# Kernel optimization log

Measured on AMD Instinct MI355X. Metric: run time of the kernel, lower is better.

Reference implementation:

```python
import jax, jax.numpy as jnp
import numpy as np

BS = 256          # batch_size
NN = BS - 1
D = 128           # projection dim
SIGMA = 0.07      # rbf gamma (self.sigma)
C = 1.0
REG = 0.1
NUM_ITERS = 1000
ETA = 0.001
USE_NORM = True


def setup_inputs() -> dict:
    key = jax.random.key(0)
    k1, k2 = jax.random.split(key)
    z = jax.random.normal(k1, (BS, 2, D), dtype=jnp.float32)
    alpha_init = jax.random.normal(k2, (BS, NN, 1), dtype=jnp.float32)
    return {"z": z, "alpha_init": alpha_init}


def _rbf_kernel(X, Y, gamma):
    # exp(-gamma * ||x - y||^2)
    xn = jnp.sum(X * X, axis=1, keepdims=True)          # [n,1]
    yn = jnp.sum(Y * Y, axis=1, keepdims=True).T        # [1,m]
    d = xn + yn - 2.0 * (X @ Y.T)
    return jnp.exp(-gamma * d)


def _pgd_nesterov(DD, p, alpha0, eta, num_iters, C, use_norm):
    # minimize 0.5 a'DDa - p'a  s.t. 0 <= a <= C, batched over bs
    def step(carry, t):
        alpha, alpha_prev = carry
        beta = t / (t + 3.0)
        y = alpha + beta * (alpha - alpha_prev)
        grad = jnp.einsum('bij,bjk->bik', DD, y) - p     # [bs,nn,1]
        if use_norm:
            grad = grad / (jnp.linalg.norm(grad, axis=1, keepdims=True) + 1e-12)
        alpha_new = jnp.clip(y - eta * grad, 0.0, C)
        return (alpha_new, alpha), None
    (alpha, _), _ = jax.lax.scan(step, (alpha0, alpha0),
                                 jnp.arange(num_iters, dtype=jnp.float32))
    return alpha


def reference(z, alpha_init):
    bs, nn = BS, NN
    # F.normalize(z, p=2, dim=1): normalize over the view axis (faithful to source)
    nrm = jnp.maximum(jnp.linalg.norm(z, axis=1, keepdims=True), 1e-12)
    ftr = z / nrm
    ftr = jnp.concatenate([ftr[:, 0, :], ftr[:, 1, :]], axis=0)   # [2bs, d]

    K = _rbf_kernel(ftr[:bs], ftr, SIGMA)                          # [bs, 2bs]

    # ---- QP construction + solve under no_grad ----
    Kd = jax.lax.stop_gradient(K)
    KK = Kd[:, :bs]                                                # block: first bs cols
    r = jnp.arange(bs)
    m = jnp.arange(nn)
    # idx[i] = [0..bs-1] without i  (KMASK row/col removal)
    idx = m[None, :] + (m[None, :] >= r[:, None]).astype(jnp.int32)  # [bs, nn]
    KK_sub = KK[idx[:, :, None], idx[:, None, :]]                  # [bs,nn,nn]
    row = jnp.take_along_axis(KK, idx, axis=1)                     # row[i,m]=KK[i,idx[i,m]]
    # Delta[i,j,k] = 1 + reg*d_jk + KK[j,k] - KK[i,j] - KK[i,k]  (j,k != i)
    DD = (1.0 + REG * jnp.eye(nn, dtype=KK.dtype)[None]
          + KK_sub - row[:, :, None] - row[:, None, :])            # [bs,nn,nn]

    p = 2.0 * jnp.ones((bs, nn, 1), dtype=jnp.float32)
    alpha0 = jnp.clip(jax.nn.relu(alpha_init), 0.0, C)
    alpha = _pgd_nesterov(DD, p, alpha0, ETA, NUM_ITERS, C, USE_NORM)
    alpha_y = jnp.clip(jax.nn.relu(alpha[:, :, 0]), 0.0, C)
    alpha_y = jax.lax.stop_gradient(alpha_y)                       # [bs,nn]
    alpha_x = alpha_y.sum(axis=1)                                  # [bs]

    # ---- loss terms (grad flows through K here) ----
    Ks = K[:, bs:]                                                 # block12: [bs,bs]
    # Kn.T[i,m] = Ks.T[i, idx[i,m]]  (neg_mask = off-diagonal)
    KnT = jnp.take_along_axis(Ks.T, idx, axis=1)                   # [bs,nn]
    pos = jnp.diagonal(Ks)                                         # pos_mask = eye
    pos_loss = jnp.mean(alpha_x * pos)
    neg_loss = jnp.sum(alpha_y * KnT) / bs
    loss = neg_loss - pos_loss

    sparsity = ((alpha_y == C).sum().astype(jnp.float32)
                / ((alpha_y > 0).sum().astype(jnp.float32) + 1e-10))
    num_zero = (alpha_y == 0.0).mean()
    return (loss, pos.mean(), KnT.mean(), sparsity, num_zero, jnp.float32(0.0))
```

## Files before the change

### kernel.cpp

```cpp
#include <hip/hip_runtime.h>
#include <math.h>

#define BS   256
#define NN   255
#define DIM  128
#define GAMMA 0.07
#define NUM_ITERS 1000

typedef float v2f __attribute__((ext_vector_type(2)));

__device__ __forceinline__ double wred_d(double v) {
  #pragma unroll
  for (int k = 1; k < 64; k <<= 1) v += __shfl_xor(v, k, 64);
  return v;
}
__device__ __forceinline__ int wred_i(int v) {
  #pragma unroll
  for (int k = 1; k < 64; k <<= 1) v += __shfl_xor(v, k, 64);
  return v;
}

__device__ __forceinline__ float RLF(float v, int lane) {
  return __int_as_float(__builtin_amdgcn_readlane(__float_as_int(v), lane));
}

template <int CTRL, int RMASK>
__device__ __forceinline__ float dpp_add(float x) {
  int t = __builtin_amdgcn_update_dpp(0, __float_as_int(x), CTRL, RMASK, 0xf, true);
  return x + __int_as_float(t);
}
__device__ __forceinline__ float wred64_dpp(float x) {
  x = dpp_add<0x111, 0xf>(x);
  x = dpp_add<0x112, 0xf>(x);
  x = dpp_add<0x114, 0xf>(x);
  x = dpp_add<0x118, 0xf>(x);
  x = dpp_add<0x142, 0xa>(x);
  x = dpp_add<0x143, 0xc>(x);
  return RLF(x, 63);
}

__device__ __forceinline__ void pk_fma(v2f& acc, const v2f& k, const v2f& y) {
  asm("v_pk_fma_f32 %0, %1, %2, %0" : "+v"(acc) : "v"(k), "v"(y));
}

__device__ __forceinline__ float rsq_nr(float x) {
  float r;
  asm("v_rsq_f32 %0, %1" : "=v"(r) : "v"(x));
  r = r * (1.5f - 0.5f * x * r * r);
  return r;
}

__global__ void k_ftr(const float* __restrict__ z, double* __restrict__ ftrT) {
  int b = blockIdx.x;
  int d = threadIdx.x;
  double z0 = (double)z[b * 256 + d];
  double z1 = (double)z[b * 256 + 128 + d];
  double n = sqrt(z0 * z0 + z1 * z1);
  n = fmax(n, 1e-12);
  ftrT[d * 512 + b]       = z0 / n;
  ftrT[d * 512 + 256 + b] = z1 / n;
}

__global__ void k_K(const double* __restrict__ ftrT, float* __restrict__ K,
                    double* __restrict__ pk_knt, double* __restrict__ pos_arr) {
  int i = blockIdx.x;
  int t = threadIdx.x;
  __shared__ double rowi[DIM];
  __shared__ double redd[4];
  if (t < DIM) rowi[t] = ftrT[t * 512 + i];
  __syncthreads();
  double xn = 0.0;
  #pragma unroll 8
  for (int d = 0; d < DIM; ++d) xn += rowi[d] * rowi[d];

  double knt_part = 0.0;
  #pragma unroll
  for (int h = 0; h < 2; ++h) {
    int j = t + h * 256;
    double dot = 0.0, sq = 0.0;
    #pragma unroll 8
    for (int d = 0; d < DIM; ++d) {
      double f = ftrT[d * 512 + j];
      dot += rowi[d] * f;
      sq  += f * f;
    }
    double dist = xn + sq - 2.0 * dot;
    double kv = exp(-GAMMA * dist);
    K[i * 512 + j] = (float)kv;
    if (h == 1) {
      if (j == 256 + i) pos_arr[i] = kv;
      else knt_part += kv;
    }
  }
  double w = wred_d(knt_part);
  if ((t & 63) == 0) redd[t >> 6] = w;
  __syncthreads();
  if (t == 0) pk_knt[i] = redd[0] + redd[1] + redd[2] + redd[3];
}

__global__ __launch_bounds__(1024, 4) void k_pgd(
    const float* __restrict__ K, const float* __restrict__ alpha_init,
    double* __restrict__ neg_arr, double* __restrict__ sa_arr,
    int* __restrict__ cnt1, int* __restrict__ cntp, int* __restrict__ cnt0) {
  int r = blockIdx.x;
  int tid = threadIdx.x;
  int l = tid & 63;
  int rg = tid >> 6;
  int rb = rg & 3;
  int cb = rg >> 2;
  int col = 64 * cb + l;

  __shared__ __align__(16) float ytil[BS];
  __shared__ __align__(16) float part[4][BS];
  __shared__ __align__(16) float grs[4];
  __shared__ float S_lds[1];
  __shared__ float betat[1024];

  betat[tid] = (float)tid / ((float)tid + 3.0f);

  v2f kp[32];
  #pragma unroll
  for (int j = 0; j < 32; ++j) {
    kp[j].x = K[(64 * rb + 2 * j + 0) * 512 + col];
    kp[j].y = K[(64 * rb + 2 * j + 1) * 512 + col];
  }
  #pragma unroll
  for (int j = 0; j < 32; ++j)
    asm volatile("" : "+v"(kp[j]));

  float al[4], ap[4], yv[4], kv[4], rm2[4];
  if (rg == 0) {
    #pragma unroll
    for (int k = 0; k < 4; ++k) {
      int a = 4 * l + k;
      if (a == r) {
        al[k] = 0.f; ap[k] = 0.f; yv[k] = 0.f; kv[k] = 0.f; rm2[k] = 0.f;
      } else {
        int c = a - (a > r ? 1 : 0);
        float v = alpha_init[r * NN + c];
        v = fminf(fmaxf(v, 0.f), 1.f);
        al[k] = v; ap[k] = v; yv[k] = v;
        kv[k] = 1.0f - K[r * 512 + a];
        rm2[k] = 2.0f;
      }
    }
    float4 y4 = {yv[0], yv[1], yv[2], yv[3]};
    *(float4*)&ytil[4 * l] = y4;
  }
  __syncthreads();

  for (int it = 0; it < NUM_ITERS; ++it) {
    if (rg == 1) {
      float4 yq = *(const float4*)&ytil[4 * l];
      float Sv = wred64_dpp((yq.x + yq.y) + (yq.z + yq.w));
      if (l == 0) S_lds[0] = Sv;
    }
    const float4* yb = (const float4*)&ytil[64 * rb];
    v2f acc = {0.f, 0.f};
    #pragma unroll
    for (int jq = 0; jq < 16; ++jq) {
      float4 yq = yb[jq];
      v2f ylo = {yq.x, yq.y};
      v2f yhi = {yq.z, yq.w};
      pk_fma(acc, kp[2 * jq + 0], ylo);
      pk_fma(acc, kp[2 * jq + 1], yhi);
    }
    float pv = acc.x + acc.y;
    part[rb][col] = pv;
    if (col == r) grs[rb] = pv;
    __syncthreads();

    if (rg == 0) {
      float4 p0 = *(const float4*)&part[0][4 * l];
      float4 p1 = *(const float4*)&part[1][4 * l];
      float4 p2 = *(const float4*)&part[2][4 * l];
      float4 p3 = *(const float4*)&part[3][4 * l];
      float4 g4 = *(const float4*)&grs[0];
      float Sv = S_lds[0];
      float beta = betat[it + 1];
      float gr = (g4.x + g4.y) + (g4.z + g4.w);
      float gA[4];
      gA[0] = (p0.x + p1.x) + (p2.x + p3.x);
      gA[1] = (p0.y + p1.y) + (p2.y + p3.y);
      gA[2] = (p0.z + p1.z) + (p2.z + p3.z);
      gA[3] = (p0.w + p1.w) + (p2.w + p3.w);
      float g[4];
      #pragma unroll
      for (int k = 0; k < 4; ++k)
        g[k] = (gA[k] - gr) - rm2[k] + kv[k] * Sv + 0.1f * yv[k];
      float n2 = wred64_dpp((g[0] * g[0] + g[1] * g[1]) + (g[2] * g[2] + g[3] * g[3]));
      float sinv = 0.001f * rsq_nr(n2);
      #pragma unroll
      for (int k = 0; k < 4; ++k) {
        float na = fminf(fmaxf(fmaf(-sinv, g[k], yv[k]), 0.f), 1.f);
        ap[k] = al[k];
        al[k] = na;
        yv[k] = fmaf(beta, na - ap[k], na);
      }
      float4 y4 = {yv[0], yv[1], yv[2], yv[3]};
      *(float4*)&ytil[4 * l] = y4;
    }
    __syncthreads();
  }

  if (rg == 0) {
    double nl = 0.0, sa = 0.0;
    int c1 = 0, cp = 0, cz = 0;
    #pragma unroll
    for (int k = 0; k < 4; ++k) {
      int a = 4 * l + k;
      if (a != r) {
        float kx = K[a * 512 + 256 + r];
        nl += (double)al[k] * (double)kx;
        sa += (double)al[k];
        c1 += (al[k] == 1.0f);
        cp += (al[k] > 0.0f);
        cz += (al[k] == 0.0f);
      }
    }
    nl = wred_d(nl); sa = wred_d(sa);
    c1 = wred_i(c1); cp = wred_i(cp); cz = wred_i(cz);
    if (l == 0) {
      neg_arr[r] = nl;
      sa_arr[r]  = sa;
      cnt1[r] = c1; cntp[r] = cp; cnt0[r] = cz;
    }
  }
}

__global__ void k_fin(const double* __restrict__ pk_knt, const double* __restrict__ pos_arr,
                      const double* __restrict__ neg_arr, const double* __restrict__ sa_arr,
                      const int* __restrict__ cnt1, const int* __restrict__ cntp,
                      const int* __restrict__ cnt0, float* __restrict__ out) {
  int t = threadIdx.x;
  __shared__ double rd[16];
  __shared__ int ri[12];
  double knt = pk_knt[t];
  double pos = pos_arr[t];
  double neg = neg_arr[t];
  double pl  = sa_arr[t] * pos_arr[t];
  int a1 = cnt1[t], ap = cntp[t], a0 = cnt0[t];
  knt = wred_d(knt); pos = wred_d(pos); neg = wred_d(neg); pl = wred_d(pl);
  a1 = wred_i(a1); ap = wred_i(ap); a0 = wred_i(a0);
  int w = t >> 6;
  if ((t & 63) == 0) {
    rd[w] = knt; rd[4 + w] = pos; rd[8 + w] = neg; rd[12 + w] = pl;
    ri[w] = a1; ri[4 + w] = ap; ri[8 + w] = a0;
  }
  __syncthreads();
  if (t == 0) {
    double kntS = rd[0] + rd[1] + rd[2] + rd[3];
    double posS = rd[4] + rd[5] + rd[6] + rd[7];
    double negS = rd[8] + rd[9] + rd[10] + rd[11];
    double plS  = rd[12] + rd[13] + rd[14] + rd[15];
    int c1t = ri[0] + ri[1] + ri[2] + ri[3];
    int cpt = ri[4] + ri[5] + ri[6] + ri[7];
    int c0t = ri[8] + ri[9] + ri[10] + ri[11];
    out[0] = (float)(negS / 256.0 - plS / 256.0);
    out[1] = (float)(posS / 256.0);
    out[2] = (float)(kntS / (256.0 * 255.0));
    out[3] = (float)c1t / ((float)cpt + 1e-10f);
    out[4] = (float)c0t / 65280.0f;
    out[5] = 0.0f;
  }
}

extern "C" void kernel_launch(void* const* d_in, const int* in_sizes, int n_in,
                              void* d_out, int out_size, void* d_ws, size_t ws_size,
                              hipStream_t stream) {
  const float* z     = (const float*)d_in[0];
  const float* ainit = (const float*)d_in[1];
  char* ws = (char*)d_ws;
  double* ftrT   = (double*)ws;
  float*  K      = (float*)(ws + 524288);
  double* pk_knt = (double*)(ws + 1048576);
  double* pos_a  = (double*)(ws + 1048576 + 2048);
  double* neg_a  = (double*)(ws + 1048576 + 4096);
  double* sa_a   = (double*)(ws + 1048576 + 6144);
  int* cnt1 = (int*)(ws + 1048576 + 8192);
  int* cntp = (int*)(ws + 1048576 + 8192 + 1024);
  int* cnt0 = (int*)(ws + 1048576 + 8192 + 2048);
  float* out = (float*)d_out;

  k_ftr<<<256, 128, 0, stream>>>(z, ftrT);
  k_K  <<<256, 256, 0, stream>>>(ftrT, K, pk_knt, pos_a);
  k_pgd<<<256, 1024, 0, stream>>>(K, ainit, neg_a, sa_a, cnt1, cntp, cnt0);
  k_fin<<<1, 256, 0, stream>>>(pk_knt, pos_a, neg_a, sa_a, cnt1, cntp, cnt0, out);
}
```

Measured before the change: 927.1 us.

## Repartition PGD matvec so each wave owns 16 K rows with float4 columns

```diff
diff --git a/kernel.cpp b/kernel.cpp
--- a/kernel.cpp
+++ b/kernel.cpp
@@ -39,15 +39,16 @@
   return RLF(x, 63);
 }
 
-__device__ __forceinline__ void pk_fma(v2f& acc, const v2f& k, const v2f& y) {
-  asm("v_pk_fma_f32 %0, %1, %2, %0" : "+v"(acc) : "v"(k), "v"(y));
-}
-
 __device__ __forceinline__ float rsq_nr(float x) {
   float r;
   asm("v_rsq_f32 %0, %1" : "=v"(r) : "v"(x));
   r = r * (1.5f - 0.5f * x * r * r);
   return r;
+}
+
+__device__ __forceinline__ float4 add4(float4 a, float4 b) {
+  float4 c; c.x = a.x + b.x; c.y = a.y + b.y; c.z = a.z + b.z; c.w = a.w + b.w;
+  return c;
 }
 
 __global__ void k_ftr(const float* __restrict__ z, double* __restrict__ ftrT) {
@@ -106,27 +107,21 @@
   int tid = threadIdx.x;
   int l = tid & 63;
   int rg = tid >> 6;
-  int rb = rg & 3;
-  int cb = rg >> 2;
-  int col = 64 * cb + l;
 
   __shared__ __align__(16) float ytil[BS];
-  __shared__ __align__(16) float part[4][BS];
-  __shared__ __align__(16) float grs[4];
+  __shared__ __align__(16) float part[16][BS];
   __shared__ float S_lds[1];
   __shared__ float betat[1024];
 
   betat[tid] = (float)tid / ((float)tid + 3.0f);
 
-  v2f kp[32];
-  #pragma unroll
-  for (int j = 0; j < 32; ++j) {
-    kp[j].x = K[(64 * rb + 2 * j + 0) * 512 + col];
-    kp[j].y = K[(64 * rb + 2 * j + 1) * 512 + col];
-  }
-  #pragma unroll
-  for (int j = 0; j < 32; ++j)
-    asm volatile("" : "+v"(kp[j]));
+  float4 kq[16];
+  #pragma unroll
+  for (int j = 0; j < 16; ++j)
+    kq[j] = *(const float4*)&K[(16 * rg + j) * 512 + 4 * l];
+  #pragma unroll
+  for (int j = 0; j < 16; ++j)
+    asm volatile("" : "+v"(kq[j].x), "+v"(kq[j].y), "+v"(kq[j].z), "+v"(kq[j].w));
 
   float al[4], ap[4], yv[4], kv[4], rm2[4];
   if (rg == 0) {
@@ -149,45 +144,64 @@
   }
   __syncthreads();
 
+  int rq = r >> 2, rc = r & 3;
+
   for (int it = 0; it < NUM_ITERS; ++it) {
     if (rg == 1) {
       float4 yq = *(const float4*)&ytil[4 * l];
       float Sv = wred64_dpp((yq.x + yq.y) + (yq.z + yq.w));
       if (l == 0) S_lds[0] = Sv;
     }
-    const float4* yb = (const float4*)&ytil[64 * rb];
-    v2f acc = {0.f, 0.f};
+    const float4* yb = (const float4*)&ytil[16 * rg];
+    float4 acc = {0.f, 0.f, 0.f, 0.f};
     #pragma unroll
-    for (int jq = 0; jq < 16; ++jq) {
-      float4 yq = yb[jq];
-      v2f ylo = {yq.x, yq.y};
-      v2f yhi = {yq.z, yq.w};
-      pk_fma(acc, kp[2 * jq + 0], ylo);
-      pk_fma(acc, kp[2 * jq + 1], yhi);
-    }
-    float pv = acc.x + acc.y;
-    part[rb][col] = pv;
-    if (col == r) grs[rb] = pv;
+    for (int jj = 0; jj < 4; ++jj) {
+      float4 yq = yb[jj];
+      float4 k0 = kq[4 * jj + 0], k1 = kq[4 * jj + 1];
+      float4 k2 = kq[4 * jj + 2], k3 = kq[4 * jj + 3];
+      acc.x = fmaf(k0.x, yq.x, acc.x); acc.y = fmaf(k0.y, yq.x, acc.y);
+      acc.z = fmaf(k0.z, yq.x, acc.z); acc.w = fmaf(k0.w, yq.x, acc.w);
+      acc.x = fmaf(k1.x, yq.y, acc.x); acc.y = fmaf(k1.y, yq.y, acc.y);
+      acc.z = fmaf(k1.z, yq.y, acc.z); acc.w = fmaf(k1.w, yq.y, acc.w);
+      acc.x = fmaf(k2.x, yq.z, acc.x); acc.y = fmaf(k2.y, yq.z, acc.y);
+      acc.z = fmaf(k2.z, yq.z, acc.z); acc.w = fmaf(k2.w, yq.z, acc.w);
+      acc.x = fmaf(k3.x, yq.w, acc.x); acc.y = fmaf(k3.y, yq.w, acc.y);
+      acc.z = fmaf(k3.z, yq.w, acc.z); acc.w = fmaf(k3.w, yq.w, acc.w);
+    }
+    *(float4*)&part[rg][4 * l] = acc;
     __syncthreads();
 
     if (rg == 0) {
-      float4 p0 = *(const float4*)&part[0][4 * l];
-      float4 p1 = *(const float4*)&part[1][4 * l];
-      float4 p2 = *(const float4*)&part[2][4 * l];
-      float4 p3 = *(const float4*)&part[3][4 * l];
-      float4 g4 = *(const float4*)&grs[0];
+      float4 q0  = *(const float4*)&part[0][4 * l];
+      float4 q1  = *(const float4*)&part[1][4 * l];
+      float4 q2  = *(const float4*)&part[2][4 * l];
+      float4 q3  = *(const float4*)&part[3][4 * l];
+      float4 q4  = *(const float4*)&part[4][4 * l];
+      float4 q5  = *(const float4*)&part[5][4 * l];
+      float4 q6  = *(const float4*)&part[6][4 * l];
+      float4 q7  = *(const float4*)&part[7][4 * l];
+      float4 q8  = *(const float4*)&part[8][4 * l];
+      float4 q9  = *(const float4*)&part[9][4 * l];
+      float4 q10 = *(const float4*)&part[10][4 * l];
+      float4 q11 = *(const float4*)&part[11][4 * l];
+      float4 q12 = *(const float4*)&part[12][4 * l];
+      float4 q13 = *(const float4*)&part[13][4 * l];
+      float4 q14 = *(const float4*)&part[14][4 * l];
+      float4 q15 = *(const float4*)&part[15][4 * l];
+      float4 s0 = add4(add4(q0, q1), add4(q2, q3));
+      float4 s1 = add4(add4(q4, q5), add4(q6, q7));
+      float4 s2 = add4(add4(q8, q9), add4(q10, q11));
+      float4 s3 = add4(add4(q12, q13), add4(q14, q15));
+      float4 gA = add4(add4(s0, s1), add4(s2, s3));
+      float grv = (rc == 0) ? gA.x : (rc == 1) ? gA.y : (rc == 2) ? gA.z : gA.w;
+      float gr = RLF(grv, rq);
       float Sv = S_lds[0];
       float beta = betat[it + 1];
-      float gr = (g4.x + g4.y) + (g4.z + g4.w);
-      float gA[4];
-      gA[0] = (p0.x + p1.x) + (p2.x + p3.x);
-      gA[1] = (p0.y + p1.y) + (p2.y + p3.y);
-      gA[2] = (p0.z + p1.z) + (p2.z + p3.z);
-      gA[3] = (p0.w + p1.w) + (p2.w + p3.w);
       float g[4];
-      #pragma unroll
-      for (int k = 0; k < 4; ++k)
-        g[k] = (gA[k] - gr) - rm2[k] + kv[k] * Sv + 0.1f * yv[k];
+      g[0] = (gA.x - gr) - rm2[0] + kv[0] * Sv + 0.1f * yv[0];
+      g[1] = (gA.y - gr) - rm2[1] + kv[1] * Sv + 0.1f * yv[1];
+      g[2] = (gA.z - gr) - rm2[2] + kv[2] * Sv + 0.1f * yv[2];
+      g[3] = (gA.w - gr) - rm2[3] + kv[3] * Sv + 0.1f * yv[3];
       float n2 = wred64_dpp((g[0] * g[0] + g[1] * g[1]) + (g[2] * g[2] + g[3] * g[3]));
       float sinv = 0.001f * rsq_nr(n2);
       #pragma unroll
```

After: 1.428 ms. 1.54x slower.
